# Kernel tuning notes

Measured on AMD Instinct MI355X. Metric: run time of the kernel, lower is better.

Reference implementation:

```python
import jax, jax.numpy as jnp
import numpy as np

EPS = 1e-12

def setup_inputs() -> dict:
    key = jax.random.key(0)
    ks = jax.random.split(key, 7)
    bs, seq, d_in, d_out = 8, 2048, 4096, 4096
    n_tasks, n_splits, n_skills, rank = 64, 1, 8, 16
    return {
        "x": jax.random.normal(ks[0], (bs, seq, d_in), dtype=jnp.float32),
        "weight": jax.random.normal(ks[1], (d_out, d_in), dtype=jnp.float32) * 0.02,
        "bias": jax.random.normal(ks[2], (d_out,), dtype=jnp.float32) * 0.02,
        "module_logits": jax.random.normal(ks[3], (n_tasks, n_splits * n_skills), dtype=jnp.float32) * 0.001,
        "lora_a": jax.random.normal(ks[4], (n_splits, n_skills, d_in // n_splits, rank), dtype=jnp.float32) * 0.02,
        "lora_b": jax.random.normal(ks[5], (n_splits, n_skills, rank, d_out // n_splits), dtype=jnp.float32) * 0.02,
        "task_ids": jax.random.randint(ks[6], (bs,), 0, n_tasks, dtype=jnp.int64),
    }

def reference(x, weight, bias, module_logits, lora_a, lora_b, task_ids):
    # Eval-mode PolytroponSelector: sigmoid then sum-normalize per split.
    n_splits, n_skills, _, rank = lora_a.shape
    bs = x.shape[0]
    mw = jax.nn.sigmoid(module_logits[task_ids]).reshape(bs, n_splits, n_skills)
    mw = mw / (mw.sum(axis=-1, keepdims=True) + EPS)
    # Mix per-skill LoRA factors: A [bs, in, rank], B [bs, rank, out]
    A = jnp.einsum('bqs,qsdr->bqdr', mw, lora_a).reshape(bs, -1, rank)
    B = jnp.einsum('bqs,qsrd->bqrd', mw, lora_b)
    B = jnp.transpose(B, (0, 2, 1, 3)).reshape(bs, rank, -1)
    # Low-rank adapter path: (x @ A) @ B / rank
    adapter = jnp.einsum('btr,bro->bto', jnp.einsum('bti,bir->btr', x, A), B) / rank
    # Base linear + adapter
    return jnp.einsum('bti,oi->bto', x, weight) + bias + adapter
```

## Files before the change

### kernel.cpp

```cpp
#include <hip/hip_runtime.h>
#include <hip/hip_bf16.h>
#include <cstdint>
#include <cstddef>

typedef __attribute__((ext_vector_type(4))) float floatx4;
typedef __attribute__((ext_vector_type(8))) __bf16 bf16x8;

#define BS 8
#define SEQ 2048
#define M_TOT 16384
#define DK 4096
#define DN 4096
#define NSK 8
#define RANK 16

__device__ __forceinline__ unsigned short f2bf(float f) {
  union { __hip_bfloat16 h; unsigned short u; } v;
  v.h = __float2bfloat16(f);
  return v.u;
}

__device__ __forceinline__ void async16(const void* g, void* l) {
  __builtin_amdgcn_global_load_lds(
      (const __attribute__((address_space(1))) unsigned int*)g,
      (__attribute__((address_space(3))) unsigned int*)l, 16, 0, 0);
}

__global__ void prep_mw_kernel(const float* __restrict__ logits,
                               const void* __restrict__ task_raw,
                               float* __restrict__ mw) {
  const int* t32 = (const int*)task_raw;
  bool is64 = true;
#pragma unroll
  for (int b = 0; b < BS; ++b)
    if (t32[2 * b + 1] != 0) is64 = false;
  int tid = threadIdx.x;
  int b = tid >> 3, s = tid & 7;
  int task = is64 ? t32[2 * b] : t32[b];
  float lg = logits[task * NSK + s];
  float sg = 1.0f / (1.0f + expf(-lg));
  float sum = sg;
  sum += __shfl_xor(sum, 1);
  sum += __shfl_xor(sum, 2);
  sum += __shfl_xor(sum, 4);
  mw[tid] = sg / (sum + 1e-12f);
}

__global__ __launch_bounds__(256) void prep_a_kernel(
    const float* __restrict__ lora_a, const float* __restrict__ mw,
    unsigned short* __restrict__ a_bft) {
  int b = blockIdx.y;
  int d = blockIdx.x * 256 + threadIdx.x;
  float w[NSK];
#pragma unroll
  for (int s = 0; s < NSK; ++s) w[s] = mw[b * NSK + s];
  float acc[RANK];
#pragma unroll
  for (int r = 0; r < RANK; ++r) acc[r] = 0.f;
  for (int s = 0; s < NSK; ++s) {
    const float4* p = (const float4*)&lora_a[((size_t)s * DK + d) * RANK];
#pragma unroll
    for (int q = 0; q < 4; ++q) {
      float4 v = p[q];
      acc[q * 4 + 0] += w[s] * v.x;
      acc[q * 4 + 1] += w[s] * v.y;
      acc[q * 4 + 2] += w[s] * v.z;
      acc[q * 4 + 3] += w[s] * v.w;
    }
  }
#pragma unroll
  for (int r = 0; r < RANK; ++r)
    a_bft[((size_t)b * RANK + r) * DK + d] = f2bf(acc[r]);
}

__global__ __launch_bounds__(256) void prep_b_kernel(
    const float* __restrict__ lora_b, const float* __restrict__ mw,
    unsigned short* __restrict__ baug) {
  int b = blockIdx.y;
  int n = blockIdx.x * 256 + threadIdx.x;
  float w[NSK];
#pragma unroll
  for (int s = 0; s < NSK; ++s) w[s] = mw[b * NSK + s];
  unsigned short ov[32];
#pragma unroll
  for (int r = 0; r < RANK; ++r) {
    float acc = 0.f;
#pragma unroll
    for (int s = 0; s < NSK; ++s)
      acc += w[s] * lora_b[((size_t)s * RANK + r) * DN + n];
    ov[r] = f2bf(acc * 0.0625f);
  }
#pragma unroll
  for (int r = RANK; r < 32; ++r) ov[r] = 0;
  uint4* dst = (uint4*)&baug[((size_t)b * DN + n) * 32];
  const uint4* sv = (const uint4*)ov;
  dst[0] = sv[0]; dst[1] = sv[1]; dst[2] = sv[2]; dst[3] = sv[3];
}

__global__ __launch_bounds__(256) void conv_f32_to_bf16(
    const float* __restrict__ src, unsigned short* __restrict__ dst,
    long long n4) {
  long long stride = (long long)gridDim.x * 256;
  for (long long i = (long long)blockIdx.x * 256 + threadIdx.x; i < n4; i += stride) {
    float4 v = ((const float4*)src)[i];
    ushort4 o;
    o.x = f2bf(v.x); o.y = f2bf(v.y); o.z = f2bf(v.z); o.w = f2bf(v.w);
    ((ushort4*)dst)[i] = o;
  }
}

__global__ __launch_bounds__(256) void t_gemm_kernel(
    const unsigned short* __restrict__ xb, const unsigned short* __restrict__ abft,
    float* __restrict__ t_f32) {
  const int wave = threadIdx.x >> 6;
  const int lane = threadIdx.x & 63;
  const int mtile = blockIdx.x * 4 + wave;
  const int row0 = mtile * 16;
  const int b = row0 >> 11;
  const int k0 = blockIdx.y * 1024;
  const int fr = lane & 15;
  const int fq = (lane >> 4) * 8;
  const unsigned short* pa = xb + (size_t)(row0 + fr) * DK + fq + k0;
  const unsigned short* pb = abft + ((size_t)b * RANK + fr) * DK + fq + k0;
  floatx4 acc = {0.f, 0.f, 0.f, 0.f};
  for (int k = 0; k < 1024; k += 32) {
    bf16x8 av = *(const bf16x8*)(pa + k);
    bf16x8 bv = *(const bf16x8*)(pb + k);
    acc = __builtin_amdgcn_mfma_f32_16x16x32_bf16(av, bv, acc, 0, 0, 0);
  }
  const int col = lane & 15;
  const int rowq = (lane >> 4) * 4;
#pragma unroll
  for (int j = 0; j < 4; ++j)
    atomicAdd(&t_f32[(size_t)(row0 + rowq + j) * RANK + col], acc[j]);
}

__global__ __launch_bounds__(256) void t_final_kernel(
    const float* __restrict__ t_f32, unsigned short* __restrict__ taug) {
  int i = blockIdx.x * 256 + threadIdx.x;
  int row = i >> 4, r = i & 15;
  taug[(size_t)row * 32 + r] = f2bf(t_f32[i]);
  taug[(size_t)row * 32 + 16 + r] = 0;
}

__global__ __launch_bounds__(512, 2) void main_gemm(
    const unsigned short* __restrict__ xb, const unsigned short* __restrict__ wb,
    const unsigned short* __restrict__ taug, const unsigned short* __restrict__ baug,
    const float* __restrict__ bias, float* __restrict__ out) {
  __shared__ __align__(1024) unsigned short lds[65536];

  const int tid = threadIdx.x;
  const int wave = tid >> 6;
  const int lane = tid & 63;
  const int wm = wave >> 2;
  const int wn = wave & 3;
  const int fr = lane & 15;
  const int fq = (lane >> 4) << 3;

  const int orig = blockIdx.x;
  const int swb = (orig & 7) * 128 + (orig >> 3);
  const int tile_m = swb >> 4;
  const int tile_n = swb & 15;
  const int m0 = tile_m * 256;
  const int n0 = tile_n * 256;
  const int batch = tile_m >> 3;

  const int laneoff = (lane >> 3) * DK + (((lane & 7) ^ (lane >> 3)) << 3);
  const unsigned short* aSrc = xb + (size_t)(m0 + 16 * wave) * DK + laneoff;
  const unsigned short* bSrc = wb + (size_t)(n0 + 16 * wave) * DK + laneoff;

#define STG_A(d, h, kt) do {                                                        \
    async16(aSrc + (size_t)(h) * (128 * DK) + ((size_t)(kt) << 6),                  \
            &lds[(d) * 32768 + (h) * 8192 + wave * 1024]);                          \
    async16(aSrc + (size_t)(h) * (128 * DK) + 8 * DK + ((size_t)(kt) << 6),         \
            &lds[(d) * 32768 + (h) * 8192 + wave * 1024 + 512]);                    \
  } while (0)
#define STG_B(d, h, kt) do {                                                        \
    async16(bSrc + (size_t)(h) * (128 * DK) + ((size_t)(kt) << 6),                  \
            &lds[(d) * 32768 + 16384 + (h) * 8192 + wave * 1024]);                  \
    async16(bSrc + (size_t)(h) * (128 * DK) + 8 * DK + ((size_t)(kt) << 6),         \
            &lds[(d) * 32768 + 16384 + (h) * 8192 + wave * 1024 + 512]);            \
  } while (0)

  const int colb0 = fq ^ ((fr & 7) << 3);
  const int colb1 = colb0 ^ 32;
  const int aRd0 = wm * 8192 + fr * 64 + colb0;
  const int aRd1 = wm * 8192 + fr * 64 + colb1;
  const int bRd0 = 16384 + wn * 4096 + fr * 64 + colb0;
  const int bRd1 = 16384 + wn * 4096 + fr * 64 + colb1;

#define RD_A(d, t, ks)                                                              \
  (*(const bf16x8*)&lds[(d) * 32768 + ((ks) ? aRd1 : aRd0) + (t) * 1024])
#define RD_B(d, u, ks)                                                              \
  (*(const bf16x8*)&lds[(d) * 32768 + ((ks) ? bRd1 : bRd0) + (u) * 1024])

  floatx4 acc[8][4];
#pragma unroll
  for (int t = 0; t < 8; ++t)
#pragma unroll
    for (int u = 0; u < 4; ++u) acc[t][u] = (floatx4){0.f, 0.f, 0.f, 0.f};

  bf16x8 a[4][2];
  bf16x8 b0[2][2];
  bf16x8 b1[2][2];

  STG_A(0, 0, 0); STG_A(0, 1, 0); STG_B(0, 0, 0); STG_B(0, 1, 0);
  STG_A(1, 0, 1); STG_A(1, 1, 1); STG_B(1, 0, 1);
  asm volatile("s_waitcnt vmcnt(6)" ::: "memory");
  __builtin_amdgcn_s_barrier();

#define TILE(d, kt) do {                                                            \
                      \
    _Pragma("unroll")                                                               \
    for (int t = 0; t < 4; ++t) { a[t][0] = RD_A(d, t, 0); a[t][1] = RD_A(d, t, 1); } \
    _Pragma("unroll")                                                               \
    for (int u = 0; u < 2; ++u) { b0[u][0] = RD_B(d, u, 0); b0[u][1] = RD_B(d, u, 1); } \
    if ((kt) + 1 < 64) STG_B(1 - (d), 1, (kt) + 1);                                 \
    __builtin_amdgcn_s_barrier();                                                   \
    asm volatile("s_waitcnt lgkmcnt(0)" ::: "memory");                              \
    __builtin_amdgcn_s_setprio(1);                                                  \
    _Pragma("unroll")                                                               \
    for (int t = 0; t < 4; ++t)                                                     \
      _Pragma("unroll")                                                             \
      for (int u = 0; u < 2; ++u) {                                                 \
        acc[t][u] = __builtin_amdgcn_mfma_f32_16x16x32_bf16(a[t][0], b0[u][0], acc[t][u], 0, 0, 0); \
        acc[t][u] = __builtin_amdgcn_mfma_f32_16x16x32_bf16(a[t][1], b0[u][1], acc[t][u], 0, 0, 0); \
      }                                                                             \
    __builtin_amdgcn_s_setprio(0);                                                  \
    __builtin_amdgcn_s_barrier();                                                   \
                                             \
    _Pragma("unroll")                                                               \
    for (int u = 0; u < 2; ++u) { b1[u][0] = RD_B(d, u + 2, 0); b1[u][1] = RD_B(d, u + 2, 1); } \
    __builtin_amdgcn_s_barrier();                                                   \
    asm volatile("s_waitcnt lgkmcnt(0)" ::: "memory");                              \
    __builtin_amdgcn_s_setprio(1);                                                  \
    _Pragma("unroll")                                                               \
    for (int t = 0; t < 4; ++t)                                                     \
      _Pragma("unroll")                                                             \
      for (int u = 0; u < 2; ++u) {                                                 \
        acc[t][u + 2] = __builtin_amdgcn_mfma_f32_16x16x32_bf16(a[t][0], b1[u][0], acc[t][u + 2], 0, 0, 0); \
        acc[t][u + 2] = __builtin_amdgcn_mfma_f32_16x16x32_bf16(a[t][1], b1[u][1], acc[t][u + 2], 0, 0, 0); \
      }                                                                             \
    __builtin_amdgcn_s_setprio(0);                                                  \
    __builtin_amdgcn_s_barrier();                                                   \
                                             \
    _Pragma("unroll")                                                               \
    for (int t = 0; t < 4; ++t) { a[t][0] = RD_A(d, t + 4, 0); a[t][1] = RD_A(d, t + 4, 1); } \
    __builtin_amdgcn_s_barrier();                                                   \
    asm volatile("s_waitcnt lgkmcnt(0)" ::: "memory");                              \
    __builtin_amdgcn_s_setprio(1);                                                  \
    _Pragma("unroll")                                                               \
    for (int t = 0; t < 4; ++t)                                                     \
      _Pragma("unroll")                                                             \
      for (int u = 0; u < 2; ++u) {                                                 \
        acc[t + 4][u] = __builtin_amdgcn_mfma_f32_16x16x32_bf16(a[t][0], b0[u][0], acc[t + 4][u], 0, 0, 0); \
        acc[t + 4][u] = __builtin_amdgcn_mfma_f32_16x16x32_bf16(a[t][1], b0[u][1], acc[t + 4][u], 0, 0, 0); \
      }                                                                             \
    __builtin_amdgcn_s_setprio(0);                                                  \
    __builtin_amdgcn_s_barrier();                                                   \
         \
        \
    if ((kt) + 2 < 64) {                                                            \
      STG_A(d, 0, (kt) + 2); STG_A(d, 1, (kt) + 2); STG_B(d, 0, (kt) + 2);          \
      asm volatile("s_waitcnt vmcnt(6)" ::: "memory");                              \
    } else {                                                                        \
      asm volatile("s_waitcnt vmcnt(0)" ::: "memory");                              \
    }                                                                               \
    __builtin_amdgcn_s_barrier();                                                   \
    __builtin_amdgcn_s_setprio(1);                                                  \
    _Pragma("unroll")                                                               \
    for (int t = 0; t < 4; ++t)                                                     \
      _Pragma("unroll")                                                             \
      for (int u = 0; u < 2; ++u) {                                                 \
        acc[t + 4][u + 2] = __builtin_amdgcn_mfma_f32_16x16x32_bf16(a[t][0], b1[u][0], acc[t + 4][u + 2], 0, 0, 0); \
        acc[t + 4][u + 2] = __builtin_amdgcn_mfma_f32_16x16x32_bf16(a[t][1], b1[u][1], acc[t + 4][u + 2], 0, 0, 0); \
      }                                                                             \
    __builtin_amdgcn_s_setprio(0);                                                  \
    __builtin_amdgcn_s_barrier();                                                   \
  } while (0)

  for (int it = 0; it < 32; ++it) {
    const int kt0 = it * 2;
    TILE(0, kt0);
    TILE(1, kt0 + 1);
  }

  {
    const unsigned short* tA = taug + (size_t)(m0 + wm * 128 + fr) * 32 + fq;
    const unsigned short* tB = baug + ((size_t)batch * DN + n0 + wn * 64 + fr) * 32 + fq;
    bf16x8 av[8], bv[4];
#pragma unroll
    for (int t = 0; t < 8; ++t) av[t] = *(const bf16x8*)(tA + (size_t)t * 512);
#pragma unroll
    for (int u = 0; u < 4; ++u) bv[u] = *(const bf16x8*)(tB + (size_t)u * 512);
#pragma unroll
    for (int t = 0; t < 8; ++t)
#pragma unroll
      for (int u = 0; u < 4; ++u)
        acc[t][u] = __builtin_amdgcn_mfma_f32_16x16x32_bf16(av[t], bv[u], acc[t][u], 0, 0, 0);
  }

  const int rowq = (lane >> 4) * 4;
#pragma unroll
  for (int u = 0; u < 4; ++u) {
    const int col = n0 + wn * 64 + u * 16 + fr;
    const float bvv = bias[col];
#pragma unroll
    for (int t = 0; t < 8; ++t) {
      float* po = out + (size_t)(m0 + wm * 128 + t * 16 + rowq) * DN + col;
#pragma unroll
      for (int j = 0; j < 4; ++j) po[(size_t)j * DN] = acc[t][u][j] + bvv;
    }
  }
#undef TILE
#undef RD_A
#undef RD_B
#undef STG_A
#undef STG_B
}

extern "C" void kernel_launch(void* const* d_in, const int* in_sizes, int n_in,
                              void* d_out, int out_size, void* d_ws, size_t ws_size,
                              hipStream_t stream) {
  (void)in_sizes; (void)n_in; (void)out_size; (void)ws_size;
  const float* x             = (const float*)d_in[0];
  const float* weight        = (const float*)d_in[1];
  const float* bias          = (const float*)d_in[2];
  const float* module_logits = (const float*)d_in[3];
  const float* lora_a        = (const float*)d_in[4];
  const float* lora_b        = (const float*)d_in[5];
  const void*  task_ids      = d_in[6];
  float* out = (float*)d_out;

  char* ws = (char*)d_ws;
  unsigned short* xb   = (unsigned short*)(ws);
  unsigned short* wb   = (unsigned short*)(ws + 134217728);
  unsigned short* taug = (unsigned short*)(ws + 167772160);
  unsigned short* baug = (unsigned short*)(ws + 168820736);
  unsigned short* abft = (unsigned short*)(ws + 170917888);
  float*          tf32 = (float*)(ws + 171966464);
  float*          mw   = (float*)(ws + 173015040);

  hipLaunchKernelGGL(prep_mw_kernel, dim3(1), dim3(64), 0, stream,
                     module_logits, task_ids, mw);
  hipLaunchKernelGGL(prep_a_kernel, dim3(16, 8), dim3(256), 0, stream,
                     lora_a, mw, abft);
  hipLaunchKernelGGL(prep_b_kernel, dim3(16, 8), dim3(256), 0, stream,
                     lora_b, mw, baug);
  hipLaunchKernelGGL(conv_f32_to_bf16, dim3(2048), dim3(256), 0, stream,
                     weight, wb, (long long)(4096LL * 4096 / 4));
  hipLaunchKernelGGL(conv_f32_to_bf16, dim3(8192), dim3(256), 0, stream,
                     x, xb, (long long)(16384LL * 4096 / 4));
  hipMemsetAsync(tf32, 0, (size_t)M_TOT * RANK * sizeof(float), stream);
  hipLaunchKernelGGL(t_gemm_kernel, dim3(256, 4), dim3(256), 0, stream,
                     xb, abft, tf32);
  hipLaunchKernelGGL(t_final_kernel, dim3(1024), dim3(256), 0, stream,
                     tf32, taug);
  hipLaunchKernelGGL(main_gemm, dim3(1024), dim3(512), 0, stream,
                     xb, wb, taug, baug, bias, out);
}
```

Baseline: 1.001 ms.

## Fuse prep kernels, drop atomics in t-GEMM, and spread main GEMM prefetches

Merges the mixing-weight, LoRA-A and LoRA-B prep into one kernel and the two fp32-to-bf16 conversions into one launch. The t-GEMM now reduces its split-K partials through shared memory instead of global atomics, which removes the memset and finalize kernels. In the main GEMM, global-to-LDS loads are issued in quarter-tile pieces spread across the compute phases, and one barrier/waitcnt stage is dropped to improve overlap. This cuts launch count and atomic traffic, with some risk of LDS hazards from the reordered prefetch timing.

```diff
diff --git a/kernel.cpp b/kernel.cpp
--- a/kernel.cpp
+++ b/kernel.cpp
@@ -26,121 +26,116 @@
       (__attribute__((address_space(3))) unsigned int*)l, 16, 0, 0);
 }
 
-__global__ void prep_mw_kernel(const float* __restrict__ logits,
-                               const void* __restrict__ task_raw,
-                               float* __restrict__ mw) {
+__device__ __forceinline__ void compute_mw(const float* __restrict__ logits,
+                                           const void* __restrict__ task_raw,
+                                           int b, float* w) {
   const int* t32 = (const int*)task_raw;
   bool is64 = true;
 #pragma unroll
-  for (int b = 0; b < BS; ++b)
-    if (t32[2 * b + 1] != 0) is64 = false;
-  int tid = threadIdx.x;
-  int b = tid >> 3, s = tid & 7;
+  for (int bb = 0; bb < BS; ++bb)
+    if (t32[2 * bb + 1] != 0) is64 = false;
   int task = is64 ? t32[2 * b] : t32[b];
-  float lg = logits[task * NSK + s];
-  float sg = 1.0f / (1.0f + expf(-lg));
-  float sum = sg;
-  sum += __shfl_xor(sum, 1);
-  sum += __shfl_xor(sum, 2);
-  sum += __shfl_xor(sum, 4);
-  mw[tid] = sg / (sum + 1e-12f);
-}
-
-__global__ __launch_bounds__(256) void prep_a_kernel(
-    const float* __restrict__ lora_a, const float* __restrict__ mw,
-    unsigned short* __restrict__ a_bft) {
+  float sum = 0.f;
+#pragma unroll
+  for (int s = 0; s < NSK; ++s) {
+    w[s] = 1.0f / (1.0f + expf(-logits[task * NSK + s]));
+    sum += w[s];
+  }
+  float inv = 1.0f / (sum + 1e-12f);
+#pragma unroll
+  for (int s = 0; s < NSK; ++s) w[s] *= inv;
+}
+
+__global__ __launch_bounds__(256) void prep_ab_kernel(
+    const float* __restrict__ lora_a, const float* __restrict__ lora_b,
+    const float* __restrict__ logits, const void* __restrict__ task_raw,
+    unsigned short* __restrict__ abft, unsigned short* __restrict__ baug) {
   int b = blockIdx.y;
-  int d = blockIdx.x * 256 + threadIdx.x;
   float w[NSK];
-#pragma unroll
-  for (int s = 0; s < NSK; ++s) w[s] = mw[b * NSK + s];
-  float acc[RANK];
-#pragma unroll
-  for (int r = 0; r < RANK; ++r) acc[r] = 0.f;
-  for (int s = 0; s < NSK; ++s) {
-    const float4* p = (const float4*)&lora_a[((size_t)s * DK + d) * RANK];
-#pragma unroll
-    for (int q = 0; q < 4; ++q) {
-      float4 v = p[q];
-      acc[q * 4 + 0] += w[s] * v.x;
-      acc[q * 4 + 1] += w[s] * v.y;
-      acc[q * 4 + 2] += w[s] * v.z;
-      acc[q * 4 + 3] += w[s] * v.w;
+  compute_mw(logits, task_raw, b, w);
+  if (blockIdx.z == 0) {
+    int d = blockIdx.x * 256 + threadIdx.x;
+    float acc[RANK];
+#pragma unroll
+    for (int r = 0; r < RANK; ++r) acc[r] = 0.f;
+    for (int s = 0; s < NSK; ++s) {
+      const float4* p = (const float4*)&lora_a[((size_t)s * DK + d) * RANK];
+#pragma unroll
+      for (int q = 0; q < 4; ++q) {
+        float4 v = p[q];
+        acc[q * 4 + 0] += w[s] * v.x;
+        acc[q * 4 + 1] += w[s] * v.y;
+        acc[q * 4 + 2] += w[s] * v.z;
+        acc[q * 4 + 3] += w[s] * v.w;
+      }
     }
-  }
-#pragma unroll
-  for (int r = 0; r < RANK; ++r)
-    a_bft[((size_t)b * RANK + r) * DK + d] = f2bf(acc[r]);
-}
-
-__global__ __launch_bounds__(256) void prep_b_kernel(
-    const float* __restrict__ lora_b, const float* __restrict__ mw,
-    unsigned short* __restrict__ baug) {
-  int b = blockIdx.y;
-  int n = blockIdx.x * 256 + threadIdx.x;
-  float w[NSK];
-#pragma unroll
-  for (int s = 0; s < NSK; ++s) w[s] = mw[b * NSK + s];
-  unsigned short ov[32];
-#pragma unroll
-  for (int r = 0; r < RANK; ++r) {
-    float acc = 0.f;
-#pragma unroll
-    for (int s = 0; s < NSK; ++s)
-      acc += w[s] * lora_b[((size_t)s * RANK + r) * DN + n];
-    ov[r] = f2bf(acc * 0.0625f);
-  }
-#pragma unroll
-  for (int r = RANK; r < 32; ++r) ov[r] = 0;
-  uint4* dst = (uint4*)&baug[((size_t)b * DN + n) * 32];
-  const uint4* sv = (const uint4*)ov;
-  dst[0] = sv[0]; dst[1] = sv[1]; dst[2] = sv[2]; dst[3] = sv[3];
-}
-
-__global__ __launch_bounds__(256) void conv_f32_to_bf16(
-    const float* __restrict__ src, unsigned short* __restrict__ dst,
-    long long n4) {
+#pragma unroll
+    for (int r = 0; r < RANK; ++r)
+      abft[((size_t)b * RANK + r) * DK + d] = f2bf(acc[r]);
+  } else {
+    int n = blockIdx.x * 256 + threadIdx.x;
+    unsigned short ov[32];
+#pragma unroll
+    for (int r = 0; r < RANK; ++r) {
+      float acc = 0.f;
+#pragma unroll
+      for (int s = 0; s < NSK; ++s)
+        acc += w[s] * lora_b[((size_t)s * RANK + r) * DN + n];
+      ov[r] = f2bf(acc * 0.0625f);
+    }
+#pragma unroll
+    for (int r = RANK; r < 32; ++r) ov[r] = 0;
+    uint4* dst = (uint4*)&baug[((size_t)b * DN + n) * 32];
+    const uint4* sv = (const uint4*)ov;
+    dst[0] = sv[0]; dst[1] = sv[1]; dst[2] = sv[2]; dst[3] = sv[3];
+  }
+}
+
+__global__ __launch_bounds__(256) void conv_all(
+    const float* __restrict__ wsrc, const float* __restrict__ xsrc,
+    unsigned short* __restrict__ wb, unsigned short* __restrict__ xb) {
+  const long long n4w = 4194304LL;
+  const long long n4t = 20971520LL;
   long long stride = (long long)gridDim.x * 256;
-  for (long long i = (long long)blockIdx.x * 256 + threadIdx.x; i < n4; i += stride) {
-    float4 v = ((const float4*)src)[i];
+  for (long long i = (long long)blockIdx.x * 256 + threadIdx.x; i < n4t;
+       i += stride) {
+    const float4* s; ushort4* d; long long j;
+    if (i < n4w) { s = (const float4*)wsrc; d = (ushort4*)wb; j = i; }
+    else         { s = (const float4*)xsrc; d = (ushort4*)xb; j = i - n4w; }
+    float4 v = s[j];
     ushort4 o;
     o.x = f2bf(v.x); o.y = f2bf(v.y); o.z = f2bf(v.z); o.w = f2bf(v.w);
-    ((ushort4*)dst)[i] = o;
+    d[j] = o;
   }
 }
 
 __global__ __launch_bounds__(256) void t_gemm_kernel(
     const unsigned short* __restrict__ xb, const unsigned short* __restrict__ abft,
-    float* __restrict__ t_f32) {
+    unsigned short* __restrict__ taug) {
+  __shared__ float red[4][256];
   const int wave = threadIdx.x >> 6;
   const int lane = threadIdx.x & 63;
-  const int mtile = blockIdx.x * 4 + wave;
-  const int row0 = mtile * 16;
+  const int row0 = blockIdx.x * 16;
   const int b = row0 >> 11;
-  const int k0 = blockIdx.y * 1024;
   const int fr = lane & 15;
   const int fq = (lane >> 4) * 8;
-  const unsigned short* pa = xb + (size_t)(row0 + fr) * DK + fq + k0;
-  const unsigned short* pb = abft + ((size_t)b * RANK + fr) * DK + fq + k0;
+  const unsigned short* pa = xb + (size_t)(row0 + fr) * DK + wave * 1024 + fq;
+  const unsigned short* pb = abft + ((size_t)b * RANK + fr) * DK + wave * 1024 + fq;
   floatx4 acc = {0.f, 0.f, 0.f, 0.f};
   for (int k = 0; k < 1024; k += 32) {
     bf16x8 av = *(const bf16x8*)(pa + k);
     bf16x8 bv = *(const bf16x8*)(pb + k);
     acc = __builtin_amdgcn_mfma_f32_16x16x32_bf16(av, bv, acc, 0, 0, 0);
   }
-  const int col = lane & 15;
   const int rowq = (lane >> 4) * 4;
 #pragma unroll
-  for (int j = 0; j < 4; ++j)
-    atomicAdd(&t_f32[(size_t)(row0 + rowq + j) * RANK + col], acc[j]);
-}
-
-__global__ __launch_bounds__(256) void t_final_kernel(
-    const float* __restrict__ t_f32, unsigned short* __restrict__ taug) {
-  int i = blockIdx.x * 256 + threadIdx.x;
-  int row = i >> 4, r = i & 15;
-  taug[(size_t)row * 32 + r] = f2bf(t_f32[i]);
-  taug[(size_t)row * 32 + 16 + r] = 0;
+  for (int j = 0; j < 4; ++j) red[wave][(rowq + j) * 16 + fr] = acc[j];
+  __syncthreads();
+  int i = threadIdx.x;
+  float v = red[0][i] + red[1][i] + red[2][i] + red[3][i];
+  int r = i >> 4, c = i & 15;
+  taug[(size_t)(row0 + r) * 32 + c] = f2bf(v);
+  taug[(size_t)(row0 + r) * 32 + 16 + c] = 0;
 }
 
 __global__ __launch_bounds__(512, 2) void main_gemm(
@@ -165,22 +160,17 @@
   const int n0 = tile_n * 256;
   const int batch = tile_m >> 3;
 
-  const int laneoff = (lane >> 3) * DK + (((lane & 7) ^ (lane >> 3)) << 3);
-  const unsigned short* aSrc = xb + (size_t)(m0 + 16 * wave) * DK + laneoff;
-  const unsigned short* bSrc = wb + (size_t)(n0 + 16 * wave) * DK + laneoff;
-
-#define STG_A(d, h, kt) do {                                                        \
-    async16(aSrc + (size_t)(h) * (128 * DK) + ((size_t)(kt) << 6),                  \
-            &lds[(d) * 32768 + (h) * 8192 + wave * 1024]);                          \
-    async16(aSrc + (size_t)(h) * (128 * DK) + 8 * DK + ((size_t)(kt) << 6),         \
-            &lds[(d) * 32768 + (h) * 8192 + wave * 1024 + 512]);                    \
-  } while (0)
-#define STG_B(d, h, kt) do {                                                        \
-    async16(bSrc + (size_t)(h) * (128 * DK) + ((size_t)(kt) << 6),                  \
-            &lds[(d) * 32768 + 16384 + (h) * 8192 + wave * 1024]);                  \
-    async16(bSrc + (size_t)(h) * (128 * DK) + 8 * DK + ((size_t)(kt) << 6),         \
-            &lds[(d) * 32768 + 16384 + (h) * 8192 + wave * 1024 + 512]);            \
-  } while (0)
+  const int lrow = lane >> 3;
+  const int lcol = (((lane & 7) ^ lrow) << 3);
+  const unsigned short* aQ = xb + (size_t)(m0 + wave * 8 + lrow) * DK + lcol;
+  const unsigned short* bQ = wb + (size_t)(n0 + wave * 8 + lrow) * DK + lcol;
+
+#define STG_AQ(d, q, kt)                                                            \
+  async16(aQ + (size_t)(q) * (64 * DK) + ((size_t)(kt) << 6),                       \
+          &lds[(d) * 32768 + (q) * 4096 + wave * 512])
+#define STG_BQ(d, q, kt)                                                            \
+  async16(bQ + (size_t)(q) * (64 * DK) + ((size_t)(kt) << 6),                       \
+          &lds[(d) * 32768 + 16384 + (q) * 4096 + wave * 512])
 
   const int colb0 = fq ^ ((fr & 7) << 3);
   const int colb1 = colb0 ^ 32;
@@ -204,18 +194,21 @@
   bf16x8 b0[2][2];
   bf16x8 b1[2][2];
 
-  STG_A(0, 0, 0); STG_A(0, 1, 0); STG_B(0, 0, 0); STG_B(0, 1, 0);
-  STG_A(1, 0, 1); STG_A(1, 1, 1); STG_B(1, 0, 1);
+  STG_AQ(0, 0, 0); STG_AQ(0, 2, 0); STG_BQ(0, 0, 0); STG_BQ(0, 1, 0);
+  STG_AQ(0, 1, 0); STG_AQ(0, 3, 0); STG_BQ(0, 2, 0); STG_BQ(0, 3, 0);
+  STG_AQ(1, 0, 1); STG_AQ(1, 2, 1); STG_BQ(1, 0, 1); STG_BQ(1, 1, 1);
+  STG_AQ(1, 1, 1); STG_AQ(1, 3, 1);
   asm volatile("s_waitcnt vmcnt(6)" ::: "memory");
   __builtin_amdgcn_s_barrier();
 
 #define TILE(d, kt) do {                                                            \
-                      \
+             \
+    if ((kt) + 1 < 64) { STG_BQ(1 - (d), 2, (kt) + 1); STG_BQ(1 - (d), 3, (kt) + 1); } \
     _Pragma("unroll")                                                               \
     for (int t = 0; t < 4; ++t) { a[t][0] = RD_A(d, t, 0); a[t][1] = RD_A(d, t, 1); } \
     _Pragma("unroll")                                                               \
     for (int u = 0; u < 2; ++u) { b0[u][0] = RD_B(d, u, 0); b0[u][1] = RD_B(d, u, 1); } \
-    if ((kt) + 1 < 64) STG_B(1 - (d), 1, (kt) + 1);                                 \
+    asm volatile("s_waitcnt lgkmcnt(8)" ::: "memory");                              \
     __builtin_amdgcn_s_barrier();                                                   \
     asm volatile("s_waitcnt lgkmcnt(0)" ::: "memory");                              \
     __builtin_amdgcn_s_setprio(1);                                                  \
@@ -228,7 +221,8 @@
       }                                                                             \
     __builtin_amdgcn_s_setprio(0);                                                  \
     __builtin_amdgcn_s_barrier();                                                   \
-                                             \
+         \
+    if ((kt) + 2 < 64) { STG_AQ(d, 0, (kt) + 2); STG_AQ(d, 2, (kt) + 2); }          \
     _Pragma("unroll")                                                               \
     for (int u = 0; u < 2; ++u) { b1[u][0] = RD_B(d, u + 2, 0); b1[u][1] = RD_B(d, u + 2, 1); } \
     __builtin_amdgcn_s_barrier();                                                   \
@@ -243,7 +237,8 @@
       }                                                                             \
     __builtin_amdgcn_s_setprio(0);                                                  \
     __builtin_amdgcn_s_barrier();                                                   \
-                                             \
+       \
+    if ((kt) + 2 < 64) { STG_BQ(d, 0, (kt) + 2); STG_BQ(d, 1, (kt) + 2); }          \
     _Pragma("unroll")                                                               \
     for (int t = 0; t < 4; ++t) { a[t][0] = RD_A(d, t + 4, 0); a[t][1] = RD_A(d, t + 4, 1); } \
     __builtin_amdgcn_s_barrier();                                                   \
@@ -259,14 +254,8 @@
     __builtin_amdgcn_s_setprio(0);                                                  \
     __builtin_amdgcn_s_barrier();                                                   \
          \
-        \
-    if ((kt) + 2 < 64) {                                                            \
-      STG_A(d, 0, (kt) + 2); STG_A(d, 1, (kt) + 2); STG_B(d, 0, (kt) + 2);          \
-      asm volatile("s_waitcnt vmcnt(6)" ::: "memory");                              \
-    } else {                                                                        \
-      asm volatile("s_waitcnt vmcnt(0)" ::: "memory");                              \
-    }                                                                               \
-    __builtin_amdgcn_s_barrier();                                                   \
+             \
+    if ((kt) + 2 < 64) { STG_AQ(d, 1, (kt) + 2); STG_AQ(d, 3, (kt) + 2); }          \
     __builtin_amdgcn_s_setprio(1);                                                  \
     _Pragma("unroll")                                                               \
     for (int t = 0; t < 4; ++t)                                                     \
@@ -276,6 +265,8 @@
         acc[t + 4][u + 2] = __builtin_amdgcn_mfma_f32_16x16x32_bf16(a[t][1], b1[u][1], acc[t + 4][u + 2], 0, 0, 0); \
       }                                                                             \
     __builtin_amdgcn_s_setprio(0);                                                  \
+    if ((kt) + 2 < 64) { asm volatile("s_waitcnt vmcnt(6)" ::: "memory"); }         \
+    else               { asm volatile("s_waitcnt vmcnt(0)" ::: "memory"); }         \
     __builtin_amdgcn_s_barrier();                                                   \
   } while (0)
 
@@ -315,8 +306,8 @@
 #undef TILE
 #undef RD_A
 #undef RD_B
-#undef STG_A
-#undef STG_B
+#undef STG_AQ
+#undef STG_BQ
 }
 
 extern "C" void kernel_launch(void* const* d_in, const int* in_sizes, int n_in,
@@ -338,24 +329,13 @@
   unsigned short* taug = (unsigned short*)(ws + 167772160);
   unsigned short* baug = (unsigned short*)(ws + 168820736);
   unsigned short* abft = (unsigned short*)(ws + 170917888);
-  float*          tf32 = (float*)(ws + 171966464);
-  float*          mw   = (float*)(ws + 173015040);
-
-  hipLaunchKernelGGL(prep_mw_kernel, dim3(1), dim3(64), 0, stream,
-                     module_logits, task_ids, mw);
-  hipLaunchKernelGGL(prep_a_kernel, dim3(16, 8), dim3(256), 0, stream,
-                     lora_a, mw, abft);
-  hipLaunchKernelGGL(prep_b_kernel, dim3(16, 8), dim3(256), 0, stream,
-                     lora_b, mw, baug);
-  hipLaunchKernelGGL(conv_f32_to_bf16, dim3(2048), dim3(256), 0, stream,
-                     weight, wb, (long long)(4096LL * 4096 / 4));
-  hipLaunchKernelGGL(conv_f32_to_bf16, dim3(8192), dim3(256), 0, stream,
-                     x, xb, (long long)(16384LL * 4096 / 4));
-  hipMemsetAsync(tf32, 0, (size_t)M_TOT * RANK * sizeof(float), stream);
-  hipLaunchKernelGGL(t_gemm_kernel, dim3(256, 4), dim3(256), 0, stream,
-                     xb, abft, tf32);
-  hipLaunchKernelGGL(t_final_kernel, dim3(1024), dim3(256), 0, stream,
-                     tf32, taug);
+
+  hipLaunchKernelGGL(prep_ab_kernel, dim3(16, 8, 2), dim3(256), 0, stream,
+                     lora_a, lora_b, module_logits, task_ids, abft, baug);
+  hipLaunchKernelGGL(conv_all, dim3(4096), dim3(256), 0, stream,
+                     weight, x, wb, xb);
+  hipLaunchKernelGGL(t_gemm_kernel, dim3(1024), dim3(256), 0, stream,
+                     xb, abft, taug);
   hipLaunchKernelGGL(main_gemm, dim3(1024), dim3(512), 0, stream,
                      xb, wb, taug, baug, bias, out);
 }
```

Result: faster. 962.9 us (-3.8%).
